# Performance work log

Hardware: AMD Instinct MI355X
Metric: run time of the kernel (lower is better)

The kernel has to match this reference:

```python
import jax, jax.numpy as jnp
import numpy as np

N_NODES = 100_000
N_EDGES = 3_200_000
F_IN, F_HID, F_OUT = 128, 128, 128
MLP_HID, MLP_OUT = 256, 64


def setup_inputs() -> dict:
    key = jax.random.key(0)
    ks = jax.random.split(key, 11)
    def w(k, shape):
        fan_in = shape[0]
        return jax.random.normal(k, shape, jnp.float32) / jnp.sqrt(jnp.float32(fan_in))
    return {
        'x':   jax.random.normal(ks[0], (N_NODES, F_IN), jnp.float32),
        'src': jax.random.randint(ks[1], (N_EDGES,), 0, N_NODES, jnp.int32),
        'dst': jax.random.randint(ks[2], (N_EDGES,), 0, N_NODES, jnp.int32),
        'w1':  w(ks[3], (F_IN, F_HID)),  'b1': jnp.zeros((F_HID,), jnp.float32),
        'w2':  w(ks[4], (F_HID, F_OUT)), 'b2': jnp.zeros((F_OUT,), jnp.float32),
        'wm1': w(ks[5], (F_OUT, MLP_HID)), 'bm1': jnp.zeros((MLP_HID,), jnp.float32),
        'wm2': w(ks[6], (MLP_HID, MLP_OUT)), 'bm2': jnp.zeros((MLP_OUT,), jnp.float32),
    }


def reference(x, src, dst, w1, b1, w2, b2, wm1, bm1, wm2, bm2):
    n = x.shape[0]
    ones = jnp.ones(src.shape[0], x.dtype)
    # DGL GraphConv norm='both': clamp degrees to >=1, symmetric D^-1/2 A D^-1/2
    out_norm = jnp.clip(jax.ops.segment_sum(ones, src, num_segments=n), 1.0) ** -0.5
    in_norm = jnp.clip(jax.ops.segment_sum(ones, dst, num_segments=n), 1.0) ** -0.5

    def gconv(h, w, b):
        msg = (h * out_norm[:, None])[src]                       # [E, F] gather
        agg = jax.ops.segment_sum(msg, dst, num_segments=n)      # [N, F] scatter-add
        return (agg * in_norm[:, None]) @ w + b

    h = jax.nn.relu(gconv(x, w1, b1))   # conv1 + relu (dropout is identity in eval)
    h = jax.nn.relu(gconv(h, w2, b2))   # conv2 + relu
    h = jax.nn.relu(h @ wm1 + bm1)      # MLP hidden layer
    return h @ wm2 + bm2                # MLP output (no final activation)
```

## Files before the change

kernel.cpp:

```cpp
#include <hip/hip_runtime.h>
#include <hip/hip_bf16.h>
#include <cstdint>

__device__ __forceinline__ unsigned short f2b(float f) {
    union { float f; unsigned int i; } v; v.f = f;
    unsigned int i = v.i;
    unsigned int r = (i + 0x7FFFu + ((i >> 16) & 1u)) >> 16;
    return (unsigned short)r;
}
__device__ __forceinline__ float b2f_lo(unsigned int p) {
    union { unsigned int i; float f; } v; v.i = p << 16; return v.f;
}
__device__ __forceinline__ float b2f_hi(unsigned int p) {
    union { unsigned int i; float f; } v; v.i = p & 0xFFFF0000u; return v.f;
}
__device__ __forceinline__ unsigned int pack2(float a, float b) {
    return (unsigned int)f2b(a) | ((unsigned int)f2b(b) << 16);
}

typedef __attribute__((__ext_vector_type__(8))) __bf16 bf16x8;
typedef __attribute__((__ext_vector_type__(4))) float  f32x4;

#define N_NODES 100000
#define N_EDGES 3200000
#define NBUCK   200
#define BSZ     500

__global__ void k_hist2(const int* __restrict__ src, const int* __restrict__ dst,
                        int* __restrict__ gcntA, int* __restrict__ gcntB, int E) {
    __shared__ int hA[NBUCK], hB[NBUCK];
    int t = threadIdx.x;
    if (t < NBUCK) { hA[t] = 0; hB[t] = 0; }
    __syncthreads();
    for (int i = blockIdx.x * blockDim.x + t; i < E; i += gridDim.x * blockDim.x) {
        atomicAdd(&hA[dst[i] / BSZ], 1);
        atomicAdd(&hB[src[i] / BSZ], 1);
    }
    __syncthreads();
    if (t < NBUCK) {
        if (hA[t]) atomicAdd(&gcntA[t], hA[t]);
        if (hB[t]) atomicAdd(&gcntB[t], hB[t]);
    }
}

__global__ void k_scan_coarse(const int* __restrict__ gcntA, const int* __restrict__ gcntB,
                              int* __restrict__ gbaseA, int* __restrict__ gbaseB,
                              int* __restrict__ gcurA, int* __restrict__ gcurB,
                              int* __restrict__ offsets) {
    __shared__ int pA[256], pB[256];
    int t = threadIdx.x;
    int vA = (t < NBUCK) ? gcntA[t] : 0;
    int vB = (t < NBUCK) ? gcntB[t] : 0;
    pA[t] = vA; pB[t] = vB;
    __syncthreads();
    for (int d = 1; d < 256; d <<= 1) {
        int a = (t >= d) ? pA[t - d] : 0;
        int b = (t >= d) ? pB[t - d] : 0;
        __syncthreads();
        pA[t] += a; pB[t] += b;
        __syncthreads();
    }
    if (t < NBUCK) {
        gbaseA[t] = pA[t] - vA; gcurA[t] = pA[t] - vA;
        gbaseB[t] = pB[t] - vB; gcurB[t] = pB[t] - vB;
    }
    if (t == 255) {
        gbaseA[NBUCK] = pA[255];
        gbaseB[NBUCK] = pB[255];
        offsets[N_NODES] = pA[255];
    }
}

__global__ void k_scatter(const int* __restrict__ src, const int* __restrict__ dst,
                          int* __restrict__ gcurA, int* __restrict__ gcurB,
                          uint2* __restrict__ pairs, int* __restrict__ keysB, int E) {
    __shared__ int hA[NBUCK], hB[NBUCK], baA[NBUCK], baB[NBUCK], lcA[NBUCK], lcB[NBUCK];
    int t = threadIdx.x;
    const int CHUNK = 12500;
    int lo = blockIdx.x * CHUNK, hi = min(lo + CHUNK, E);
    if (t < NBUCK) { hA[t] = 0; hB[t] = 0; }
    __syncthreads();
    for (int i = lo + t; i < hi; i += 256) {
        atomicAdd(&hA[dst[i] / BSZ], 1);
        atomicAdd(&hB[src[i] / BSZ], 1);
    }
    __syncthreads();
    if (t < NBUCK) {
        baA[t] = hA[t] ? atomicAdd(&gcurA[t], hA[t]) : 0;
        lcA[t] = 0;
        baB[t] = hB[t] ? atomicAdd(&gcurB[t], hB[t]) : 0;
        lcB[t] = 0;
    }
    __syncthreads();
    for (int i = lo + t; i < hi; i += 256) {
        int s = src[i], d = dst[i];
        int bA = d / BSZ;
        int l  = atomicAdd(&lcA[bA], 1);
        pairs[baA[bA] + l] = make_uint2((unsigned)s, (unsigned)d);
        int bB = s / BSZ;
        int l2 = atomicAdd(&lcB[bB], 1);
        keysB[baB[bB] + l2] = s;
    }
}

__global__ void k_csr_bucket(const uint2* __restrict__ pairs, const int* __restrict__ gbaseA,
                             int* __restrict__ offsets, float* __restrict__ in_norm,
                             int* __restrict__ esrc) {
    __shared__ int hist[512], scan[512], curs[512];
    int b = blockIdx.x, t = threadIdx.x;
    int node0 = b * BSZ;
    int bstart = gbaseA[b], bend = gbaseA[b + 1];
    if (t < 512) hist[t] = 0;
    __syncthreads();
    for (int i = bstart + t; i < bend; i += 1024)
        atomicAdd(&hist[(int)pairs[i].y - node0], 1);
    __syncthreads();
    if (t < 512) scan[t] = hist[t];
    __syncthreads();
    for (int d = 1; d < 512; d <<= 1) {
        int v = (t < 512 && t >= d) ? scan[t - d] : 0;
        __syncthreads();
        if (t < 512) scan[t] += v;
        __syncthreads();
    }
    if (t < BSZ) {
        int excl = scan[t] - hist[t];
        offsets[node0 + t] = bstart + excl;
        in_norm[node0 + t] = rsqrtf((float)max(hist[t], 1));
        curs[t] = excl;
    }
    __syncthreads();
    for (int i = bstart + t; i < bend; i += 1024) {
        uint2 p = pairs[i];
        int d = (int)p.y - node0;
        int l = atomicAdd(&curs[d], 1);
        esrc[bstart + l] = (int)p.x;
    }
}

__global__ void k_sortwave(const int* __restrict__ offsets, int* __restrict__ esrc, int N) {
    int node = blockIdx.x * 4 + (threadIdx.x >> 6);
    if (node >= N) return;
    int lane = threadIdx.x & 63;
    int lo = offsets[node], hi = offsets[node + 1];
    int len = hi - lo;
    if (len <= 1) return;
    const int INF = 0x7FFFFFFF;
    int v0 = (lane < len) ? esrc[lo + lane] : INF;
    int v1 = (64 + lane < len) ? esrc[lo + 64 + lane] : INF;
#pragma unroll
    for (int k = 2; k <= 128; k <<= 1) {
#pragma unroll
        for (int d = 64; d > 0; d >>= 1) {
            if (d >= k) continue;
            if (d == 64) {
                int a = min(v0, v1), b = max(v0, v1);
                v0 = a; v1 = b;
            } else {
                int w0 = __shfl_xor(v0, d, 64);
                int w1 = __shfl_xor(v1, d, 64);
                bool up0 = ((lane & k) == 0);
                bool up1 = (((64 + lane) & k) == 0);
                bool lower = ((lane & d) == 0);
                v0 = (lower == up0) ? min(v0, w0) : max(v0, w0);
                v1 = (lower == up1) ? min(v1, w1) : max(v1, w1);
            }
        }
    }
    if (lane < len) esrc[lo + lane] = v0;
    if (64 + lane < len) esrc[lo + 64 + lane] = v1;
}

__global__ void k_count_bucket(const int* __restrict__ keys, const int* __restrict__ gbaseB,
                               float* __restrict__ out_norm) {
    __shared__ int hist[512];
    int b = blockIdx.x, t = threadIdx.x;
    int node0 = b * BSZ;
    int bstart = gbaseB[b], bend = gbaseB[b + 1];
    if (t < 512) hist[t] = 0;
    __syncthreads();
    for (int i = bstart + t; i < bend; i += 1024)
        atomicAdd(&hist[keys[i] - node0], 1);
    __syncthreads();
    if (t < BSZ) out_norm[node0 + t] = rsqrtf((float)max(hist[t], 1));
}

__global__ void k_scale(const float4* __restrict__ x4, const float* __restrict__ out_norm,
                        uint2* __restrict__ xs, int total4) {
    int i = blockIdx.x * blockDim.x + threadIdx.x;
    if (i < total4) {
        int node = i >> 5;
        float on = out_norm[node];
        float4 v = x4[i];
        uint2 o;
        o.x = pack2(v.x * on, v.y * on);
        o.y = pack2(v.z * on, v.w * on);
        xs[i] = o;
    }
}

__global__ void k_transpose4(const float* __restrict__ w1, const float* __restrict__ w2,
                             const float* __restrict__ wm1, const float* __restrict__ wm2,
                             unsigned short* __restrict__ t1, unsigned short* __restrict__ t2,
                             unsigned short* __restrict__ tm1, unsigned short* __restrict__ tm2) {
    int i = blockIdx.x * blockDim.x + threadIdx.x;
    const float* w; unsigned short* t; int N, idx;
    if (i < 16384)       { w = w1;  t = t1;  N = 128; idx = i; }
    else if (i < 32768)  { w = w2;  t = t2;  N = 128; idx = i - 16384; }
    else if (i < 65536)  { w = wm1; t = tm1; N = 256; idx = i - 32768; }
    else if (i < 81920)  { w = wm2; t = tm2; N = 64;  idx = i - 65536; }
    else return;
    int K = (i < 65536) ? 128 : 256;
    int k = idx / N, n = idx - k * N;
    t[(size_t)n * K + k] = f2b(w[idx]);
}

#define AGG_NODE_BODY(node)                                                     \
    int lo = offsets[node], hi = offsets[node + 1];                             \
    float a0 = 0.f, a1 = 0.f, a2 = 0.f, a3 = 0.f,                               \
          a4 = 0.f, a5 = 0.f, a6 = 0.f, a7 = 0.f;                               \
    int k = lo + g;                                                             \
    for (; k + 12 < hi; k += 16) {                                              \
        int s0 = esrc[k];                                                       \
        int s1 = esrc[k + 4];                                                   \
        int s2 = esrc[k + 8];                                                   \
        int s3 = esrc[k + 12];                                                  \
        uint4 p0 = feat[(size_t)s0 * 16 + c];                                   \
        uint4 p1 = feat[(size_t)s1 * 16 + c];                                   \
        uint4 p2 = feat[(size_t)s2 * 16 + c];                                   \
        uint4 p3 = feat[(size_t)s3 * 16 + c];                                   \
        a0 += b2f_lo(p0.x); a1 += b2f_hi(p0.x);                                 \
        a2 += b2f_lo(p0.y); a3 += b2f_hi(p0.y);                                 \
        a4 += b2f_lo(p0.z); a5 += b2f_hi(p0.z);                                 \
        a6 += b2f_lo(p0.w); a7 += b2f_hi(p0.w);                                 \
        a0 += b2f_lo(p1.x); a1 += b2f_hi(p1.x);                                 \
        a2 += b2f_lo(p1.y); a3 += b2f_hi(p1.y);                                 \
        a4 += b2f_lo(p1.z); a5 += b2f_hi(p1.z);                                 \
        a6 += b2f_lo(p1.w); a7 += b2f_hi(p1.w);                                 \
        a0 += b2f_lo(p2.x); a1 += b2f_hi(p2.x);                                 \
        a2 += b2f_lo(p2.y); a3 += b2f_hi(p2.y);                                 \
        a4 += b2f_lo(p2.z); a5 += b2f_hi(p2.z);                                 \
        a6 += b2f_lo(p2.w); a7 += b2f_hi(p2.w);                                 \
        a0 += b2f_lo(p3.x); a1 += b2f_hi(p3.x);                                 \
        a2 += b2f_lo(p3.y); a3 += b2f_hi(p3.y);                                 \
        a4 += b2f_lo(p3.z); a5 += b2f_hi(p3.z);                                 \
        a6 += b2f_lo(p3.w); a7 += b2f_hi(p3.w);                                 \
    }                                                                           \
    for (; k < hi; k += 4) {                                                    \
        int s = esrc[k];                                                        \
        uint4 p = feat[(size_t)s * 16 + c];                                     \
        a0 += b2f_lo(p.x); a1 += b2f_hi(p.x);                                   \
        a2 += b2f_lo(p.y); a3 += b2f_hi(p.y);                                   \
        a4 += b2f_lo(p.z); a5 += b2f_hi(p.z);                                   \
        a6 += b2f_lo(p.w); a7 += b2f_hi(p.w);                                   \
    }                                                                           \
    a0 += __shfl_xor(a0, 16, 64); a0 += __shfl_xor(a0, 32, 64);                 \
    a1 += __shfl_xor(a1, 16, 64); a1 += __shfl_xor(a1, 32, 64);                 \
    a2 += __shfl_xor(a2, 16, 64); a2 += __shfl_xor(a2, 32, 64);                 \
    a3 += __shfl_xor(a3, 16, 64); a3 += __shfl_xor(a3, 32, 64);                 \
    a4 += __shfl_xor(a4, 16, 64); a4 += __shfl_xor(a4, 32, 64);                 \
    a5 += __shfl_xor(a5, 16, 64); a5 += __shfl_xor(a5, 32, 64);                 \
    a6 += __shfl_xor(a6, 16, 64); a6 += __shfl_xor(a6, 32, 64);                 \
    a7 += __shfl_xor(a7, 16, 64); a7 += __shfl_xor(a7, 32, 64);

__global__ void k_conv(const int* __restrict__ offsets, const int* __restrict__ esrc,
                       const uint4* __restrict__ feat, const float* __restrict__ in_norm,
                       const unsigned short* __restrict__ WT, const float* __restrict__ bias,
                       const float* __restrict__ row_scale, unsigned short* __restrict__ C,
                       int N) {
    __shared__ unsigned short A[32][136];
    int wv = threadIdx.x >> 6, lane = threadIdx.x & 63;
    int row0 = blockIdx.x * 32;
    int g = lane >> 4, c = lane & 15;

    for (int i = 0; i < 8; ++i) {
        int nl = wv * 8 + i;
        int node = row0 + nl;
        AGG_NODE_BODY(node)
        if (g == 0) {
            float inn = in_norm[node];
            uint4 o;
            o.x = pack2(a0 * inn, a1 * inn);
            o.y = pack2(a2 * inn, a3 * inn);
            o.z = pack2(a4 * inn, a5 * inn);
            o.w = pack2(a6 * inn, a7 * inn);
            *(uint4*)&A[nl][c * 8] = o;
        }
    }
    __syncthreads();

    int m = lane & 15, q = lane >> 4;
    const unsigned short* b0 = WT + (size_t)(wv * 32 + m) * 128 + q * 8;
    const unsigned short* b1 = b0 + (size_t)16 * 128;
    f32x4 acc00 = {0.f, 0.f, 0.f, 0.f}, acc10 = {0.f, 0.f, 0.f, 0.f};
    f32x4 acc01 = {0.f, 0.f, 0.f, 0.f}, acc11 = {0.f, 0.f, 0.f, 0.f};
#pragma unroll
    for (int k = 0; k < 128; k += 32) {
        bf16x8 bf0 = *(const bf16x8*)(b0 + k);
        bf16x8 bf1 = *(const bf16x8*)(b1 + k);
        bf16x8 af0 = *(const bf16x8*)&A[m][q * 8 + k];
        bf16x8 af1 = *(const bf16x8*)&A[16 + m][q * 8 + k];
        acc00 = __builtin_amdgcn_mfma_f32_16x16x32_bf16(af0, bf0, acc00, 0, 0, 0);
        acc10 = __builtin_amdgcn_mfma_f32_16x16x32_bf16(af1, bf0, acc10, 0, 0, 0);
        acc01 = __builtin_amdgcn_mfma_f32_16x16x32_bf16(af0, bf1, acc01, 0, 0, 0);
        acc11 = __builtin_amdgcn_mfma_f32_16x16x32_bf16(af1, bf1, acc11, 0, 0, 0);
    }
    int col0 = wv * 32 + m;
    int col1 = col0 + 16;
    float bc0 = bias[col0], bc1 = bias[col1];
#pragma unroll
    for (int r = 0; r < 4; r++) {
        int rr = row0 + q * 4 + r;
        int rr1 = rr + 16;
        float v00 = fmaxf(acc00[r] + bc0, 0.f);
        float v10 = fmaxf(acc10[r] + bc0, 0.f);
        float v01 = fmaxf(acc01[r] + bc1, 0.f);
        float v11 = fmaxf(acc11[r] + bc1, 0.f);
        if (row_scale) {
            float s0 = row_scale[rr], s1 = row_scale[rr1];
            v00 *= s0; v01 *= s0; v10 *= s1; v11 *= s1;
        }
        C[(size_t)rr * 128 + col0]  = f2b(v00);
        C[(size_t)rr * 128 + col1]  = f2b(v01);
        C[(size_t)rr1 * 128 + col0] = f2b(v10);
        C[(size_t)rr1 * 128 + col1] = f2b(v11);
    }
}

__global__ void k_conv2_mlp(const int* __restrict__ offsets, const int* __restrict__ esrc,
                            const uint4* __restrict__ feat, const float* __restrict__ in_norm,
                            const unsigned short* __restrict__ WT2, const float* __restrict__ b2,
                            const unsigned short* __restrict__ WTM1, const float* __restrict__ bm1,
                            const unsigned short* __restrict__ WTM2, const float* __restrict__ bm2,
                            float* __restrict__ out, int N) {
    __shared__ unsigned short smem[12800];
    unsigned short (*H1)[136] = (unsigned short(*)[136])(smem);
    unsigned short (*A)[136]  = (unsigned short(*)[136])(smem + 4352);
    unsigned short (*H2)[264] = (unsigned short(*)[264])(smem + 4352);

    int wv = threadIdx.x >> 6, lane = threadIdx.x & 63;
    int row0 = blockIdx.x * 32;
    int g = lane >> 4, c = lane & 15;

    for (int i = 0; i < 8; ++i) {
        int nl = wv * 8 + i;
        int node = row0 + nl;
        AGG_NODE_BODY(node)
        if (g == 0) {
            float inn = in_norm[node];
            uint4 o;
            o.x = pack2(a0 * inn, a1 * inn);
            o.y = pack2(a2 * inn, a3 * inn);
            o.z = pack2(a4 * inn, a5 * inn);
            o.w = pack2(a6 * inn, a7 * inn);
            *(uint4*)&A[nl][c * 8] = o;
        }
    }
    __syncthreads();

    int m = lane & 15, q = lane >> 4;

    {
        const unsigned short* b0 = WT2 + (size_t)(wv * 32 + m) * 128 + q * 8;
        const unsigned short* b1 = b0 + (size_t)16 * 128;
        f32x4 acc00 = {0.f, 0.f, 0.f, 0.f}, acc10 = {0.f, 0.f, 0.f, 0.f};
        f32x4 acc01 = {0.f, 0.f, 0.f, 0.f}, acc11 = {0.f, 0.f, 0.f, 0.f};
#pragma unroll
        for (int k = 0; k < 128; k += 32) {
            bf16x8 bf0 = *(const bf16x8*)(b0 + k);
            bf16x8 bf1 = *(const bf16x8*)(b1 + k);
            bf16x8 af0 = *(const bf16x8*)&A[m][q * 8 + k];
            bf16x8 af1 = *(const bf16x8*)&A[16 + m][q * 8 + k];
            acc00 = __builtin_amdgcn_mfma_f32_16x16x32_bf16(af0, bf0, acc00, 0, 0, 0);
            acc10 = __builtin_amdgcn_mfma_f32_16x16x32_bf16(af1, bf0, acc10, 0, 0, 0);
            acc01 = __builtin_amdgcn_mfma_f32_16x16x32_bf16(af0, bf1, acc01, 0, 0, 0);
            acc11 = __builtin_amdgcn_mfma_f32_16x16x32_bf16(af1, bf1, acc11, 0, 0, 0);
        }
        __syncthreads();
        int col0 = wv * 32 + m;
        int col1 = col0 + 16;
        float bc0 = b2[col0], bc1 = b2[col1];
#pragma unroll
        for (int r = 0; r < 4; r++) {
            int rl = q * 4 + r;
            H1[rl][col0]      = f2b(fmaxf(acc00[r] + bc0, 0.f));
            H1[rl][col1]      = f2b(fmaxf(acc01[r] + bc1, 0.f));
            H1[rl + 16][col0] = f2b(fmaxf(acc10[r] + bc0, 0.f));
            H1[rl + 16][col1] = f2b(fmaxf(acc11[r] + bc1, 0.f));
        }
    }
    __syncthreads();

#pragma unroll
    for (int cb = 0; cb < 4; cb++) {
        int colh = wv * 64 + cb * 16 + m;
        const unsigned short* bp = WTM1 + (size_t)colh * 128 + q * 8;
        f32x4 acc0 = {0.f, 0.f, 0.f, 0.f};
        f32x4 acc1 = {0.f, 0.f, 0.f, 0.f};
#pragma unroll
        for (int s = 0; s < 4; s++) {
            bf16x8 bfr = *(const bf16x8*)(bp + s * 32);
            bf16x8 ha0 = *(const bf16x8*)&H1[m][s * 32 + q * 8];
            bf16x8 ha1 = *(const bf16x8*)&H1[m + 16][s * 32 + q * 8];
            acc0 = __builtin_amdgcn_mfma_f32_16x16x32_bf16(ha0, bfr, acc0, 0, 0, 0);
            acc1 = __builtin_amdgcn_mfma_f32_16x16x32_bf16(ha1, bfr, acc1, 0, 0, 0);
        }
        float bc = bm1[colh];
#pragma unroll
        for (int r = 0; r < 4; r++) {
            H2[q * 4 + r][colh]      = f2b(fmaxf(acc0[r] + bc, 0.f));
            H2[q * 4 + r + 16][colh] = f2b(fmaxf(acc1[r] + bc, 0.f));
        }
    }
    __syncthreads();

    {
        int colo = wv * 16 + m;
        const unsigned short* bp2 = WTM2 + (size_t)colo * 256 + q * 8;
        f32x4 acc0 = {0.f, 0.f, 0.f, 0.f};
        f32x4 acc1 = {0.f, 0.f, 0.f, 0.f};
#pragma unroll
        for (int s = 0; s < 8; s++) {
            bf16x8 bfr = *(const bf16x8*)(bp2 + s * 32);
            bf16x8 ha0 = *(const bf16x8*)&H2[m][s * 32 + q * 8];
            bf16x8 ha1 = *(const bf16x8*)&H2[m + 16][s * 32 + q * 8];
            acc0 = __builtin_amdgcn_mfma_f32_16x16x32_bf16(ha0, bfr, acc0, 0, 0, 0);
            acc1 = __builtin_amdgcn_mfma_f32_16x16x32_bf16(ha1, bfr, acc1, 0, 0, 0);
        }
        float bc = bm2[colo];
#pragma unroll
        for (int r = 0; r < 4; r++) {
            out[(size_t)(row0 + q * 4 + r) * 64 + colo]      = acc0[r] + bc;
            out[(size_t)(row0 + q * 4 + r + 16) * 64 + colo] = acc1[r] + bc;
        }
    }
}

extern "C" void kernel_launch(void* const* d_in, const int* in_sizes, int n_in,
                              void* d_out, int out_size, void* d_ws, size_t ws_size,
                              hipStream_t stream) {
    const float* x    = (const float*)d_in[0];
    const int*   src  = (const int*)d_in[1];
    const int*   dst  = (const int*)d_in[2];
    const float* w1   = (const float*)d_in[3];
    const float* b1   = (const float*)d_in[4];
    const float* w2   = (const float*)d_in[5];
    const float* b2   = (const float*)d_in[6];
    const float* wm1  = (const float*)d_in[7];
    const float* bm1  = (const float*)d_in[8];
    const float* wm2  = (const float*)d_in[9];
    const float* bm2  = (const float*)d_in[10];

    const int N = N_NODES;
    const int E = N_EDGES;

    char* p = (char*)d_ws;
    auto alloc = [&](size_t bytes) -> void* {
        void* r = (void*)p;
        p += (bytes + 255) & ~(size_t)255;
        return r;
    };
    int*   gcntA   = (int*)alloc(256 * 4);
    int*   gcntB   = (int*)alloc(256 * 4);
    int*   gbaseA  = (int*)alloc(256 * 4);
    int*   gbaseB  = (int*)alloc(256 * 4);
    int*   gcurA   = (int*)alloc(256 * 4);
    int*   gcurB   = (int*)alloc(256 * 4);
    int*   offsets = (int*)alloc((size_t)(N + 1) * 4);
    float* out_norm = (float*)alloc((size_t)N * 4);
    float* in_norm  = (float*)alloc((size_t)N * 4);
    int*   esrc     = (int*)alloc((size_t)E * 4);
    unsigned int* bufA = (unsigned int*)alloc((size_t)N * 128 * 2);
    unsigned int* bufB = (unsigned int*)alloc((size_t)N * 128 * 2);
    unsigned int* bufC = (unsigned int*)alloc((size_t)N * 128 * 2);
    unsigned short* wt1  = (unsigned short*)alloc(128 * 128 * 2);
    unsigned short* wt2  = (unsigned short*)alloc(128 * 128 * 2);
    unsigned short* wtm1 = (unsigned short*)alloc(256 * 128 * 2);
    unsigned short* wtm2 = (unsigned short*)alloc(64 * 256 * 2);
    (void)ws_size; (void)n_in; (void)in_sizes; (void)out_size;

    uint2* pairs = (uint2*)bufB;
    int*   keysB = (int*)bufC;

    hipMemsetAsync(gcntA, 0, 256 * 4, stream);
    hipMemsetAsync(gcntB, 0, 256 * 4, stream);

    const int TB = 256;
    k_hist2<<<dim3(256), dim3(TB), 0, stream>>>(src, dst, gcntA, gcntB, E);
    k_scan_coarse<<<dim3(1), dim3(TB), 0, stream>>>(gcntA, gcntB, gbaseA, gbaseB,
                                                    gcurA, gcurB, offsets);
    k_scatter<<<dim3(256), dim3(TB), 0, stream>>>(src, dst, gcurA, gcurB, pairs, keysB, E);
    k_csr_bucket<<<dim3(NBUCK), dim3(1024), 0, stream>>>(pairs, gbaseA, offsets, in_norm, esrc);
    k_sortwave<<<dim3(N / 4), dim3(TB), 0, stream>>>(offsets, esrc, N);
    k_count_bucket<<<dim3(NBUCK), dim3(1024), 0, stream>>>(keysB, gbaseB, out_norm);

    k_scale<<<dim3((N * 32 + TB - 1) / TB), dim3(TB), 0, stream>>>(
        (const float4*)x, out_norm, (uint2*)bufA, N * 32);
    k_transpose4<<<dim3(320), dim3(TB), 0, stream>>>(w1, w2, wm1, wm2, wt1, wt2, wtm1, wtm2);

    k_conv<<<dim3(N / 32), dim3(TB), 0, stream>>>(
        offsets, esrc, (const uint4*)bufA, in_norm, wt1, b1, out_norm,
        (unsigned short*)bufC, N);

    k_conv2_mlp<<<dim3(N / 32), dim3(TB), 0, stream>>>(
        offsets, esrc, (const uint4*)bufC, in_norm, wt2, b2, wtm1, bm1, wtm2, bm2,
        (float*)d_out, N);
}
```

Before: 599.9 us.

## Pack edge pairs, fuse count with scale, deepen gather unroll, shrink MLP smem

Each (src,dst) pair is packed into one 32-bit word holding the local dst and the src, which halves the bucket scatter traffic. The out-degree count kernel is fused with the feature scaling kernel to drop a launch and a re-read of out_norm. The aggregation loop gains a 32-edge unrolled stage so more gathers are in flight. The MLP hidden layer is computed in two halves so the H2 shared buffer shrinks, and launch bounds are added to both conv kernels to raise occupancy. The extra barriers and higher register pressure could offset some of this.

```diff
diff --git a/kernel.cpp b/kernel.cpp
--- a/kernel.cpp
+++ b/kernel.cpp
@@ -73,7 +73,7 @@
 
 __global__ void k_scatter(const int* __restrict__ src, const int* __restrict__ dst,
                           int* __restrict__ gcurA, int* __restrict__ gcurB,
-                          uint2* __restrict__ pairs, int* __restrict__ keysB, int E) {
+                          unsigned* __restrict__ pairs, int* __restrict__ keysB, int E) {
     __shared__ int hA[NBUCK], hB[NBUCK], baA[NBUCK], baB[NBUCK], lcA[NBUCK], lcB[NBUCK];
     int t = threadIdx.x;
     const int CHUNK = 12500;
@@ -96,14 +96,14 @@
         int s = src[i], d = dst[i];
         int bA = d / BSZ;
         int l  = atomicAdd(&lcA[bA], 1);
-        pairs[baA[bA] + l] = make_uint2((unsigned)s, (unsigned)d);
+        pairs[baA[bA] + l] = ((unsigned)(d - bA * BSZ) << 17) | (unsigned)s;
         int bB = s / BSZ;
         int l2 = atomicAdd(&lcB[bB], 1);
         keysB[baB[bB] + l2] = s;
     }
 }
 
-__global__ void k_csr_bucket(const uint2* __restrict__ pairs, const int* __restrict__ gbaseA,
+__global__ void k_csr_bucket(const unsigned* __restrict__ pairs, const int* __restrict__ gbaseA,
                              int* __restrict__ offsets, float* __restrict__ in_norm,
                              int* __restrict__ esrc) {
     __shared__ int hist[512], scan[512], curs[512];
@@ -113,7 +113,7 @@
     if (t < 512) hist[t] = 0;
     __syncthreads();
     for (int i = bstart + t; i < bend; i += 1024)
-        atomicAdd(&hist[(int)pairs[i].y - node0], 1);
+        atomicAdd(&hist[pairs[i] >> 17], 1);
     __syncthreads();
     if (t < 512) scan[t] = hist[t];
     __syncthreads();
@@ -131,10 +131,10 @@
     }
     __syncthreads();
     for (int i = bstart + t; i < bend; i += 1024) {
-        uint2 p = pairs[i];
-        int d = (int)p.y - node0;
+        unsigned p = pairs[i];
+        int d = (int)(p >> 17);
         int l = atomicAdd(&curs[d], 1);
-        esrc[bstart + l] = (int)p.x;
+        esrc[bstart + l] = (int)(p & 0x1FFFFu);
     }
 }
 
@@ -171,9 +171,11 @@
     if (64 + lane < len) esrc[lo + 64 + lane] = v1;
 }
 
-__global__ void k_count_bucket(const int* __restrict__ keys, const int* __restrict__ gbaseB,
-                               float* __restrict__ out_norm) {
+__global__ void k_count_scale(const int* __restrict__ keys, const int* __restrict__ gbaseB,
+                              const float4* __restrict__ x4, float* __restrict__ out_norm,
+                              uint2* __restrict__ xs) {
     __shared__ int hist[512];
+    __shared__ float onl[BSZ];
     int b = blockIdx.x, t = threadIdx.x;
     int node0 = b * BSZ;
     int bstart = gbaseB[b], bend = gbaseB[b + 1];
@@ -182,20 +184,20 @@
     for (int i = bstart + t; i < bend; i += 1024)
         atomicAdd(&hist[keys[i] - node0], 1);
     __syncthreads();
-    if (t < BSZ) out_norm[node0 + t] = rsqrtf((float)max(hist[t], 1));
-}
-
-__global__ void k_scale(const float4* __restrict__ x4, const float* __restrict__ out_norm,
-                        uint2* __restrict__ xs, int total4) {
-    int i = blockIdx.x * blockDim.x + threadIdx.x;
-    if (i < total4) {
-        int node = i >> 5;
-        float on = out_norm[node];
-        float4 v = x4[i];
+    if (t < BSZ) {
+        float on = rsqrtf((float)max(hist[t], 1));
+        onl[t] = on;
+        out_norm[node0 + t] = on;
+    }
+    __syncthreads();
+    size_t base4 = (size_t)node0 * 32;
+    for (int i = t; i < BSZ * 32; i += 1024) {
+        float on = onl[i >> 5];
+        float4 v = x4[base4 + i];
         uint2 o;
         o.x = pack2(v.x * on, v.y * on);
         o.y = pack2(v.z * on, v.w * on);
-        xs[i] = o;
+        xs[base4 + i] = o;
     }
 }
 
@@ -215,11 +217,33 @@
     t[(size_t)n * K + k] = f2b(w[idx]);
 }
 
+#define AGG_ADD(p)                                                              \
+        a0 += b2f_lo(p.x); a1 += b2f_hi(p.x);                                   \
+        a2 += b2f_lo(p.y); a3 += b2f_hi(p.y);                                   \
+        a4 += b2f_lo(p.z); a5 += b2f_hi(p.z);                                   \
+        a6 += b2f_lo(p.w); a7 += b2f_hi(p.w);
+
 #define AGG_NODE_BODY(node)                                                     \
     int lo = offsets[node], hi = offsets[node + 1];                             \
     float a0 = 0.f, a1 = 0.f, a2 = 0.f, a3 = 0.f,                               \
           a4 = 0.f, a5 = 0.f, a6 = 0.f, a7 = 0.f;                               \
     int k = lo + g;                                                             \
+    for (; k + 28 < hi; k += 32) {                                              \
+        int s0 = esrc[k];      int s1 = esrc[k + 4];                            \
+        int s2 = esrc[k + 8];  int s3 = esrc[k + 12];                           \
+        int s4 = esrc[k + 16]; int s5 = esrc[k + 20];                           \
+        int s6 = esrc[k + 24]; int s7 = esrc[k + 28];                           \
+        uint4 p0 = feat[(size_t)s0 * 16 + c];                                   \
+        uint4 p1 = feat[(size_t)s1 * 16 + c];                                   \
+        uint4 p2 = feat[(size_t)s2 * 16 + c];                                   \
+        uint4 p3 = feat[(size_t)s3 * 16 + c];                                   \
+        uint4 p4 = feat[(size_t)s4 * 16 + c];                                   \
+        uint4 p5 = feat[(size_t)s5 * 16 + c];                                   \
+        uint4 p6 = feat[(size_t)s6 * 16 + c];                                   \
+        uint4 p7 = feat[(size_t)s7 * 16 + c];                                   \
+        AGG_ADD(p0) AGG_ADD(p1) AGG_ADD(p2) AGG_ADD(p3)                         \
+        AGG_ADD(p4) AGG_ADD(p5) AGG_ADD(p6) AGG_ADD(p7)                         \
+    }                                                                           \
     for (; k + 12 < hi; k += 16) {                                              \
         int s0 = esrc[k];                                                       \
         int s1 = esrc[k + 4];                                                   \
@@ -229,30 +253,12 @@
         uint4 p1 = feat[(size_t)s1 * 16 + c];                                   \
         uint4 p2 = feat[(size_t)s2 * 16 + c];                                   \
         uint4 p3 = feat[(size_t)s3 * 16 + c];                                   \
-        a0 += b2f_lo(p0.x); a1 += b2f_hi(p0.x);                                 \
-        a2 += b2f_lo(p0.y); a3 += b2f_hi(p0.y);                                 \
-        a4 += b2f_lo(p0.z); a5 += b2f_hi(p0.z);                                 \
-        a6 += b2f_lo(p0.w); a7 += b2f_hi(p0.w);                                 \
-        a0 += b2f_lo(p1.x); a1 += b2f_hi(p1.x);                                 \
-        a2 += b2f_lo(p1.y); a3 += b2f_hi(p1.y);                                 \
-        a4 += b2f_lo(p1.z); a5 += b2f_hi(p1.z);                                 \
-        a6 += b2f_lo(p1.w); a7 += b2f_hi(p1.w);                                 \
-        a0 += b2f_lo(p2.x); a1 += b2f_hi(p2.x);                                 \
-        a2 += b2f_lo(p2.y); a3 += b2f_hi(p2.y);                                 \
-        a4 += b2f_lo(p2.z); a5 += b2f_hi(p2.z);                                 \
-        a6 += b2f_lo(p2.w); a7 += b2f_hi(p2.w);                                 \
-        a0 += b2f_lo(p3.x); a1 += b2f_hi(p3.x);                                 \
-        a2 += b2f_lo(p3.y); a3 += b2f_hi(p3.y);                                 \
-        a4 += b2f_lo(p3.z); a5 += b2f_hi(p3.z);                                 \
-        a6 += b2f_lo(p3.w); a7 += b2f_hi(p3.w);                                 \
+        AGG_ADD(p0) AGG_ADD(p1) AGG_ADD(p2) AGG_ADD(p3)                         \
     }                                                                           \
     for (; k < hi; k += 4) {                                                    \
         int s = esrc[k];                                                        \
         uint4 p = feat[(size_t)s * 16 + c];                                     \
-        a0 += b2f_lo(p.x); a1 += b2f_hi(p.x);                                   \
-        a2 += b2f_lo(p.y); a3 += b2f_hi(p.y);                                   \
-        a4 += b2f_lo(p.z); a5 += b2f_hi(p.z);                                   \
-        a6 += b2f_lo(p.w); a7 += b2f_hi(p.w);                                   \
+        AGG_ADD(p)                                                              \
     }                                                                           \
     a0 += __shfl_xor(a0, 16, 64); a0 += __shfl_xor(a0, 32, 64);                 \
     a1 += __shfl_xor(a1, 16, 64); a1 += __shfl_xor(a1, 32, 64);                 \
@@ -263,11 +269,12 @@
     a6 += __shfl_xor(a6, 16, 64); a6 += __shfl_xor(a6, 32, 64);                 \
     a7 += __shfl_xor(a7, 16, 64); a7 += __shfl_xor(a7, 32, 64);
 
-__global__ void k_conv(const int* __restrict__ offsets, const int* __restrict__ esrc,
-                       const uint4* __restrict__ feat, const float* __restrict__ in_norm,
-                       const unsigned short* __restrict__ WT, const float* __restrict__ bias,
-                       const float* __restrict__ row_scale, unsigned short* __restrict__ C,
-                       int N) {
+__global__ __launch_bounds__(256, 8)
+void k_conv(const int* __restrict__ offsets, const int* __restrict__ esrc,
+            const uint4* __restrict__ feat, const float* __restrict__ in_norm,
+            const unsigned short* __restrict__ WT, const float* __restrict__ bias,
+            const float* __restrict__ row_scale, unsigned short* __restrict__ C,
+            int N) {
     __shared__ unsigned short A[32][136];
     int wv = threadIdx.x >> 6, lane = threadIdx.x & 63;
     int row0 = blockIdx.x * 32;
@@ -316,10 +323,8 @@
         float v10 = fmaxf(acc10[r] + bc0, 0.f);
         float v01 = fmaxf(acc01[r] + bc1, 0.f);
         float v11 = fmaxf(acc11[r] + bc1, 0.f);
-        if (row_scale) {
-            float s0 = row_scale[rr], s1 = row_scale[rr1];
-            v00 *= s0; v01 *= s0; v10 *= s1; v11 *= s1;
-        }
+        float s0 = row_scale[rr], s1 = row_scale[rr1];
+        v00 *= s0; v01 *= s0; v10 *= s1; v11 *= s1;
         C[(size_t)rr * 128 + col0]  = f2b(v00);
         C[(size_t)rr * 128 + col1]  = f2b(v01);
         C[(size_t)rr1 * 128 + col0] = f2b(v10);
@@ -327,16 +332,17 @@
     }
 }
 
-__global__ void k_conv2_mlp(const int* __restrict__ offsets, const int* __restrict__ esrc,
-                            const uint4* __restrict__ feat, const float* __restrict__ in_norm,
-                            const unsigned short* __restrict__ WT2, const float* __restrict__ b2,
-                            const unsigned short* __restrict__ WTM1, const float* __restrict__ bm1,
-                            const unsigned short* __restrict__ WTM2, const float* __restrict__ bm2,
-                            float* __restrict__ out, int N) {
-    __shared__ unsigned short smem[12800];
+__global__ __launch_bounds__(256, 8)
+void k_conv2_mlp(const int* __restrict__ offsets, const int* __restrict__ esrc,
+                 const uint4* __restrict__ feat, const float* __restrict__ in_norm,
+                 const unsigned short* __restrict__ WT2, const float* __restrict__ b2,
+                 const unsigned short* __restrict__ WTM1, const float* __restrict__ bm1,
+                 const unsigned short* __restrict__ WTM2, const float* __restrict__ bm2,
+                 float* __restrict__ out, int N) {
+    __shared__ unsigned short smem[8704];
     unsigned short (*H1)[136] = (unsigned short(*)[136])(smem);
     unsigned short (*A)[136]  = (unsigned short(*)[136])(smem + 4352);
-    unsigned short (*H2)[264] = (unsigned short(*)[264])(smem + 4352);
+    unsigned short (*H2)[136] = (unsigned short(*)[136])(smem + 4352);
 
     int wv = threadIdx.x >> 6, lane = threadIdx.x & 63;
     int row0 = blockIdx.x * 32;
@@ -361,14 +367,14 @@
     int m = lane & 15, q = lane >> 4;
 
     {
-        const unsigned short* b0 = WT2 + (size_t)(wv * 32 + m) * 128 + q * 8;
-        const unsigned short* b1 = b0 + (size_t)16 * 128;
+        const unsigned short* bb0 = WT2 + (size_t)(wv * 32 + m) * 128 + q * 8;
+        const unsigned short* bb1 = bb0 + (size_t)16 * 128;
         f32x4 acc00 = {0.f, 0.f, 0.f, 0.f}, acc10 = {0.f, 0.f, 0.f, 0.f};
         f32x4 acc01 = {0.f, 0.f, 0.f, 0.f}, acc11 = {0.f, 0.f, 0.f, 0.f};
 #pragma unroll
         for (int k = 0; k < 128; k += 32) {
-            bf16x8 bf0 = *(const bf16x8*)(b0 + k);
-            bf16x8 bf1 = *(const bf16x8*)(b1 + k);
+            bf16x8 bf0 = *(const bf16x8*)(bb0 + k);
+            bf16x8 bf1 = *(const bf16x8*)(bb1 + k);
             bf16x8 af0 = *(const bf16x8*)&A[m][q * 8 + k];
             bf16x8 af1 = *(const bf16x8*)&A[16 + m][q * 8 + k];
             acc00 = __builtin_amdgcn_mfma_f32_16x16x32_bf16(af0, bf0, acc00, 0, 0, 0);
@@ -376,7 +382,6 @@
             acc01 = __builtin_amdgcn_mfma_f32_16x16x32_bf16(af0, bf1, acc01, 0, 0, 0);
             acc11 = __builtin_amdgcn_mfma_f32_16x16x32_bf16(af1, bf1, acc11, 0, 0, 0);
         }
-        __syncthreads();
         int col0 = wv * 32 + m;
         int col1 = col0 + 16;
         float bc0 = b2[col0], bc1 = b2[col1];
@@ -391,48 +396,50 @@
     }
     __syncthreads();
 
-#pragma unroll
-    for (int cb = 0; cb < 4; cb++) {
-        int colh = wv * 64 + cb * 16 + m;
-        const unsigned short* bp = WTM1 + (size_t)colh * 128 + q * 8;
-        f32x4 acc0 = {0.f, 0.f, 0.f, 0.f};
-        f32x4 acc1 = {0.f, 0.f, 0.f, 0.f};
+    f32x4 macc0 = {0.f, 0.f, 0.f, 0.f}, macc1 = {0.f, 0.f, 0.f, 0.f};
+    int colo = wv * 16 + m;
+    const unsigned short* bp2 = WTM2 + (size_t)colo * 256 + q * 8;
+#pragma unroll
+    for (int half = 0; half < 2; ++half) {
+#pragma unroll
+        for (int cb = 0; cb < 2; cb++) {
+            int colh = half * 128 + wv * 32 + cb * 16 + m;
+            const unsigned short* bp = WTM1 + (size_t)colh * 128 + q * 8;
+            f32x4 acc0 = {0.f, 0.f, 0.f, 0.f};
+            f32x4 acc1 = {0.f, 0.f, 0.f, 0.f};
+#pragma unroll
+            for (int s = 0; s < 4; s++) {
+                bf16x8 bfr = *(const bf16x8*)(bp + s * 32);
+                bf16x8 ha0 = *(const bf16x8*)&H1[m][s * 32 + q * 8];
+                bf16x8 ha1 = *(const bf16x8*)&H1[m + 16][s * 32 + q * 8];
+                acc0 = __builtin_amdgcn_mfma_f32_16x16x32_bf16(ha0, bfr, acc0, 0, 0, 0);
+                acc1 = __builtin_amdgcn_mfma_f32_16x16x32_bf16(ha1, bfr, acc1, 0, 0, 0);
+            }
+            float bc = bm1[colh];
+            int cl = colh & 127;
+#pragma unroll
+            for (int r = 0; r < 4; r++) {
+                H2[q * 4 + r][cl]      = f2b(fmaxf(acc0[r] + bc, 0.f));
+                H2[q * 4 + r + 16][cl] = f2b(fmaxf(acc1[r] + bc, 0.f));
+            }
+        }
+        __syncthreads();
 #pragma unroll
         for (int s = 0; s < 4; s++) {
-            bf16x8 bfr = *(const bf16x8*)(bp + s * 32);
-            bf16x8 ha0 = *(const bf16x8*)&H1[m][s * 32 + q * 8];
-            bf16x8 ha1 = *(const bf16x8*)&H1[m + 16][s * 32 + q * 8];
-            acc0 = __builtin_amdgcn_mfma_f32_16x16x32_bf16(ha0, bfr, acc0, 0, 0, 0);
-            acc1 = __builtin_amdgcn_mfma_f32_16x16x32_bf16(ha1, bfr, acc1, 0, 0, 0);
-        }
-        float bc = bm1[colh];
-#pragma unroll
-        for (int r = 0; r < 4; r++) {
-            H2[q * 4 + r][colh]      = f2b(fmaxf(acc0[r] + bc, 0.f));
-            H2[q * 4 + r + 16][colh] = f2b(fmaxf(acc1[r] + bc, 0.f));
-        }
-    }
-    __syncthreads();
-
-    {
-        int colo = wv * 16 + m;
-        const unsigned short* bp2 = WTM2 + (size_t)colo * 256 + q * 8;
-        f32x4 acc0 = {0.f, 0.f, 0.f, 0.f};
-        f32x4 acc1 = {0.f, 0.f, 0.f, 0.f};
-#pragma unroll
-        for (int s = 0; s < 8; s++) {
-            bf16x8 bfr = *(const bf16x8*)(bp2 + s * 32);
+            bf16x8 bfr = *(const bf16x8*)(bp2 + half * 128 + s * 32);
             bf16x8 ha0 = *(const bf16x8*)&H2[m][s * 32 + q * 8];
             bf16x8 ha1 = *(const bf16x8*)&H2[m + 16][s * 32 + q * 8];
-            acc0 = __builtin_amdgcn_mfma_f32_16x16x32_bf16(ha0, bfr, acc0, 0, 0, 0);
-            acc1 = __builtin_amdgcn_mfma_f32_16x16x32_bf16(ha1, bfr, acc1, 0, 0, 0);
-        }
-        float bc = bm2[colo];
-#pragma unroll
-        for (int r = 0; r < 4; r++) {
-            out[(size_t)(row0 + q * 4 + r) * 64 + colo]      = acc0[r] + bc;
-            out[(size_t)(row0 + q * 4 + r + 16) * 64 + colo] = acc1[r] + bc;
-        }
+            macc0 = __builtin_amdgcn_mfma_f32_16x16x32_bf16(ha0, bfr, macc0, 0, 0, 0);
+            macc1 = __builtin_amdgcn_mfma_f32_16x16x32_bf16(ha1, bfr, macc1, 0, 0, 0);
+        }
+        __syncthreads();
+    }
+
+    float bc = bm2[colo];
+#pragma unroll
+    for (int r = 0; r < 4; r++) {
+        out[(size_t)(row0 + q * 4 + r) * 64 + colo]      = macc0[r] + bc;
+        out[(size_t)(row0 + q * 4 + r + 16) * 64 + colo] = macc1[r] + bc;
     }
 }
 
@@ -479,11 +486,10 @@
     unsigned short* wtm2 = (unsigned short*)alloc(64 * 256 * 2);
     (void)ws_size; (void)n_in; (void)in_sizes; (void)out_size;
 
-    uint2* pairs = (uint2*)bufB;
-    int*   keysB = (int*)bufC;
-
-    hipMemsetAsync(gcntA, 0, 256 * 4, stream);
-    hipMemsetAsync(gcntB, 0, 256 * 4, stream);
+    unsigned* pairs = (unsigned*)bufB;
+    int*      keysB = (int*)bufC;
+
+    hipMemsetAsync(gcntA, 0, 2 * 256 * 4, stream);
 
     const int TB = 256;
     k_hist2<<<dim3(256), dim3(TB), 0, stream>>>(src, dst, gcntA, gcntB, E);
@@ -492,10 +498,9 @@
     k_scatter<<<dim3(256), dim3(TB), 0, stream>>>(src, dst, gcurA, gcurB, pairs, keysB, E);
     k_csr_bucket<<<dim3(NBUCK), dim3(1024), 0, stream>>>(pairs, gbaseA, offsets, in_norm, esrc);
     k_sortwave<<<dim3(N / 4), dim3(TB), 0, stream>>>(offsets, esrc, N);
-    k_count_bucket<<<dim3(NBUCK), dim3(1024), 0, stream>>>(keysB, gbaseB, out_norm);
-
-    k_scale<<<dim3((N * 32 + TB - 1) / TB), dim3(TB), 0, stream>>>(
-        (const float4*)x, out_norm, (uint2*)bufA, N * 32);
+    k_count_scale<<<dim3(NBUCK), dim3(1024), 0, stream>>>(
+        keysB, gbaseB, (const float4*)x, out_norm, (uint2*)bufA);
+
     k_transpose4<<<dim3(320), dim3(TB), 0, stream>>>(w1, w2, wm1, wm2, wt1, wt2, wtm1, wtm2);
 
     k_conv<<<dim3(N / 32), dim3(TB), 0, stream>>>(
```

Measured after the change: 784.5 us. 30.8% more time.
